# Optimization experiments

Measured on AMD Instinct MI355X. Metric: run time of the kernel, lower is better.

The kernel has to match this reference:

```python
import math
import jax, jax.numpy as jnp
import numpy as np

B, T, C, H = 2, 4096, 512, 8  # batch, seq_len, n_embd, n_head
D = C // H                    # head_dim = 64

def setup_inputs() -> dict:
    key = jax.random.key(0)
    k1, k2, k3 = jax.random.split(key, 3)
    x = jax.random.normal(k1, (B, T, C), dtype=jnp.float32)
    # torch Linear(C, 3C, bias=False): y = x @ W.T; we store the transposed
    # weight directly so the forward is x @ W_attn.
    W_attn = jax.random.normal(k2, (C, 3 * C), dtype=jnp.float32) * 0.02
    W_proj = jax.random.normal(k3, (C, C), dtype=jnp.float32) * 0.02
    return {"x": x, "W_attn": W_attn, "W_proj": W_proj}

def reference(x, W_attn, W_proj):
    b, t, c = x.shape
    # fused QKV projection, split like .split(n_embd, dim=2)
    qkv = x @ W_attn                              # [B,T,3C]
    q, k, v = jnp.split(qkv, 3, axis=-1)          # each [B,T,C]
    def to_heads(u):
        return u.reshape(b, t, H, D).transpose(0, 2, 1, 3)  # [B,H,T,D]
    q, k, v = to_heads(q), to_heads(k), to_heads(v)
    scale = 1.0 / math.sqrt(D)
    att = jnp.einsum('bhqd,bhkd->bhqk', q, k) * scale       # [B,H,T,T]
    causal = jnp.tril(jnp.ones((t, t), dtype=bool))         # masked_fill(triu(...,1), -inf)
    att = jnp.where(causal, att, -jnp.inf)
    probs = jax.nn.softmax(att, axis=-1)
    y = jnp.einsum('bhqk,bhkd->bhqd', probs, v)             # [B,H,T,D]
    y = y.transpose(0, 2, 1, 3).reshape(b, t, c)            # [B,T,C]
    return y @ W_proj
```

## Files before the change

kernel.cpp:

```cpp
#include <hip/hip_runtime.h>
#include <hip/hip_bf16.h>
#include <stdint.h>


typedef __attribute__((ext_vector_type(8))) short short8;
typedef __attribute__((ext_vector_type(4))) float floatx4;

__device__ __forceinline__ unsigned short f2bf(float f) {
    unsigned int x = __float_as_uint(f);
    unsigned int r = x + 0x7fffu + ((x >> 16) & 1u);
    return (unsigned short)(r >> 16);
}

__global__ __launch_bounds__(256) void transpose_w(
    const float* __restrict__ W, unsigned short* __restrict__ Wt, int Kdim, int Ndim)
{
    __shared__ unsigned short tile[32][34];
    const int tid = threadIdx.x;
    const int tx = tid & 31, ty = tid >> 5;
    const int n0 = blockIdx.x * 32, k0 = blockIdx.y * 32;
    #pragma unroll
    for (int p = 0; p < 4; ++p) {
        int k = k0 + ty + p * 8;
        tile[tx][ty + p * 8] = f2bf(W[(size_t)k * Ndim + n0 + tx]);
    }
    __syncthreads();
    #pragma unroll
    for (int p = 0; p < 4; ++p) {
        int n = n0 + ty + p * 8;
        Wt[(size_t)n * Kdim + k0 + tx] = tile[ty + p * 8][tx];
    }
}

template<int EPI, bool AF32>
__global__ __launch_bounds__(256) void mm_bt(
    const void* __restrict__ Ap,
    const unsigned short* __restrict__ Bt,
    void* __restrict__ outp)
{
    __shared__ __align__(16) unsigned short Al[128][40];
    __shared__ __align__(16) unsigned short Bl[128][40];

    const int tid  = threadIdx.x;
    const int wave = tid >> 6;
    const int lane = tid & 63;
    const int quad = lane >> 4;
    const int l16  = lane & 15;
    const int wr   = wave >> 1;
    const int wc   = wave & 1;
    const int n0 = blockIdx.x * 128;
    const int m0 = blockIdx.y * 128;

    floatx4 acc[4][4];
    #pragma unroll
    for (int i = 0; i < 4; ++i)
        #pragma unroll
        for (int j = 0; j < 4; ++j) acc[i][j] = (floatx4){0.f, 0.f, 0.f, 0.f};

    const int row = tid >> 1;
    const int cb  = (tid & 1) * 16;

    for (int k0 = 0; k0 < 512; k0 += 32) {
        __syncthreads();
        if (AF32) {
            const float* src = (const float*)Ap + (size_t)(m0 + row) * 512 + k0 + cb;
            float4 f0 = *reinterpret_cast<const float4*>(src);
            float4 f1 = *reinterpret_cast<const float4*>(src + 4);
            float4 f2 = *reinterpret_cast<const float4*>(src + 8);
            float4 f3 = *reinterpret_cast<const float4*>(src + 12);
            unsigned short o[16] = {
                f2bf(f0.x), f2bf(f0.y), f2bf(f0.z), f2bf(f0.w),
                f2bf(f1.x), f2bf(f1.y), f2bf(f1.z), f2bf(f1.w),
                f2bf(f2.x), f2bf(f2.y), f2bf(f2.z), f2bf(f2.w),
                f2bf(f3.x), f2bf(f3.y), f2bf(f3.z), f2bf(f3.w)};
            *reinterpret_cast<uint4*>(&Al[row][cb])     = reinterpret_cast<uint4*>(o)[0];
            *reinterpret_cast<uint4*>(&Al[row][cb + 8]) = reinterpret_cast<uint4*>(o)[1];
        } else {
            const unsigned short* src = (const unsigned short*)Ap + (size_t)(m0 + row) * 512 + k0 + cb;
            *reinterpret_cast<uint4*>(&Al[row][cb])     = *reinterpret_cast<const uint4*>(src);
            *reinterpret_cast<uint4*>(&Al[row][cb + 8]) = *reinterpret_cast<const uint4*>(src + 8);
        }
        {
            const unsigned short* src = &Bt[(size_t)(n0 + row) * 512 + k0 + cb];
            *reinterpret_cast<uint4*>(&Bl[row][cb])     = *reinterpret_cast<const uint4*>(src);
            *reinterpret_cast<uint4*>(&Bl[row][cb + 8]) = *reinterpret_cast<const uint4*>(src + 8);
        }
        __syncthreads();

        short8 af[4], bf[4];
        #pragma unroll
        for (int ti = 0; ti < 4; ++ti)
            af[ti] = *reinterpret_cast<const short8*>(&Al[wr * 64 + ti * 16 + l16][quad * 8]);
        #pragma unroll
        for (int tj = 0; tj < 4; ++tj)
            bf[tj] = *reinterpret_cast<const short8*>(&Bl[wc * 64 + tj * 16 + l16][quad * 8]);
        #pragma unroll
        for (int ti = 0; ti < 4; ++ti)
            #pragma unroll
            for (int tj = 0; tj < 4; ++tj)
                acc[ti][tj] = __builtin_amdgcn_mfma_f32_16x16x32_bf16(af[ti], bf[tj], acc[ti][tj], 0, 0, 0);
    }

    if (EPI == 0) {
        unsigned short* WS = (unsigned short*)outp;
        unsigned short* Qb  = WS;
        unsigned short* Kb  = WS + 4194304;
        unsigned short* Vtb = WS + 8388608;
        const int which = n0 >> 9;
        const int h = ((n0 + wc * 64) >> 6) & 7;
        const float sc = (which == 0) ? 0.18033688f : 1.0f;
        #pragma unroll
        for (int ti = 0; ti < 4; ++ti) {
            #pragma unroll
            for (int r = 0; r < 4; ++r) {
                int m = m0 + wr * 64 + ti * 16 + quad * 4 + r;
                int b = m >> 12, t = m & 4095;
                int bh = b * 8 + h;
                #pragma unroll
                for (int tj = 0; tj < 4; ++tj) {
                    int d = tj * 16 + l16;
                    unsigned short val = f2bf(acc[ti][tj][r] * sc);
                    if (which == 0)      Qb[((size_t)bh * 4096 + t) * 64 + d] = val;
                    else if (which == 1) Kb[((size_t)bh * 4096 + t) * 64 + d] = val;
                    else                 Vtb[((size_t)bh * 64 + d) * 4096 + t] = val;
                }
            }
        }
    } else {
        float* Out = (float*)outp;
        #pragma unroll
        for (int ti = 0; ti < 4; ++ti) {
            #pragma unroll
            for (int r = 0; r < 4; ++r) {
                int m = m0 + wr * 64 + ti * 16 + quad * 4 + r;
                #pragma unroll
                for (int tj = 0; tj < 4; ++tj) {
                    int n = n0 + wc * 64 + tj * 16 + l16;
                    Out[(size_t)m * 512 + n] = acc[ti][tj][r];
                }
            }
        }
    }
}

__global__ __launch_bounds__(256) void attn_mfma(
    const unsigned short* __restrict__ Q,
    const unsigned short* __restrict__ K,
    const unsigned short* __restrict__ Vt,
    unsigned short* __restrict__ Y)
{
    __shared__ __align__(16) unsigned short Kc[64][72];
    __shared__ __align__(16) unsigned short Vc[64][72];
    __shared__ __align__(16) unsigned short Pc[4][16][72];

    const int tid  = threadIdx.x;
    const int wave = tid >> 6;
    const int lane = tid & 63;
    const int quad = lane >> 4;
    const int l16  = lane & 15;

    const int bid = blockIdx.x;
    const int bh = bid & 15;
    const int j  = (bid >> 4) & 15;
    const int g  = bid >> 8;
    const int qb = (g == 0) ? j : (g == 1) ? (63 - j) : (g == 2) ? (16 + j) : (47 - j);
    const int m0 = qb * 64;

    const unsigned short* Qp = Q  + (size_t)bh * (4096 * 64);
    const unsigned short* Kp = K  + (size_t)bh * (4096 * 64);
    const unsigned short* Vp = Vt + (size_t)bh * (64 * 4096);

    const int qrow = m0 + wave * 16 + l16;
    short8 qf[2];
    qf[0] = *reinterpret_cast<const short8*>(&Qp[(size_t)qrow * 64 + quad * 8]);
    qf[1] = *reinterpret_cast<const short8*>(&Qp[(size_t)qrow * 64 + 32 + quad * 8]);

    short8 ones;
    #pragma unroll
    for (int i = 0; i < 8; ++i) ones[i] = (short)0x3F80;

    floatx4 o[4] = {{0,0,0,0},{0,0,0,0},{0,0,0,0},{0,0,0,0}};
    floatx4 o4 = {0, 0, 0, 0};

    const int r0 = tid >> 3,          c0 = (tid & 7) * 8;
    const int r1 = (tid + 256) >> 3,  c1 = c0;

    uint4 rk0 = *reinterpret_cast<const uint4*>(&Kp[(size_t)r0 * 64 + c0]);
    uint4 rk1 = *reinterpret_cast<const uint4*>(&Kp[(size_t)r1 * 64 + c1]);
    uint4 rv0 = *reinterpret_cast<const uint4*>(&Vp[(size_t)r0 * 4096 + c0]);
    uint4 rv1 = *reinterpret_cast<const uint4*>(&Vp[(size_t)r1 * 4096 + c1]);

    for (int kt = 0; kt <= qb; ++kt) {
        __syncthreads();
        *reinterpret_cast<uint4*>(&Kc[r0][c0]) = rk0;
        *reinterpret_cast<uint4*>(&Kc[r1][c1]) = rk1;
        *reinterpret_cast<uint4*>(&Vc[r0][c0]) = rv0;
        *reinterpret_cast<uint4*>(&Vc[r1][c1]) = rv1;
        __syncthreads();

        if (kt < qb) {
            const int jn = (kt + 1) * 64;
            rk0 = *reinterpret_cast<const uint4*>(&Kp[(size_t)(jn + r0) * 64 + c0]);
            rk1 = *reinterpret_cast<const uint4*>(&Kp[(size_t)(jn + r1) * 64 + c1]);
            rv0 = *reinterpret_cast<const uint4*>(&Vp[(size_t)r0 * 4096 + jn + c0]);
            rv1 = *reinterpret_cast<const uint4*>(&Vp[(size_t)r1 * 4096 + jn + c1]);
        }

        float sv[4][4];
        #pragma unroll
        for (int ct = 0; ct < 4; ++ct) {
            floatx4 s = {0, 0, 0, 0};
            #pragma unroll
            for (int kk = 0; kk < 2; ++kk) {
                short8 a = *reinterpret_cast<const short8*>(&Kc[ct * 16 + l16][kk * 32 + quad * 8]);
                s = __builtin_amdgcn_mfma_f32_16x16x32_bf16(a, qf[kk], s, 0, 0, 0);
            }
            sv[ct][0] = s[0]; sv[ct][1] = s[1]; sv[ct][2] = s[2]; sv[ct][3] = s[3];
        }

        if (kt == qb) {
            #pragma unroll
            for (int ct = 0; ct < 4; ++ct)
                #pragma unroll
                for (int r = 0; r < 4; ++r) {
                    int keyl = ct * 16 + quad * 4 + r;
                    int ql   = wave * 16 + l16;
                    sv[ct][r] = (keyl <= ql) ? sv[ct][r] : -1e30f;
                }
        }
        #pragma unroll
        for (int ct = 0; ct < 4; ++ct)
            #pragma unroll
            for (int r = 0; r < 4; ++r)
                sv[ct][r] = __builtin_amdgcn_exp2f(sv[ct][r]);

        #pragma unroll
        for (int ct = 0; ct < 4; ++ct) {
            unsigned int d0 = (unsigned int)f2bf(sv[ct][0]) | ((unsigned int)f2bf(sv[ct][1]) << 16);
            unsigned int d1 = (unsigned int)f2bf(sv[ct][2]) | ((unsigned int)f2bf(sv[ct][3]) << 16);
            *reinterpret_cast<uint2*>(&Pc[wave][l16][ct * 16 + quad * 4]) = make_uint2(d0, d1);
        }

        short8 pa[2];
        pa[0] = *reinterpret_cast<const short8*>(&Pc[wave][l16][quad * 8]);
        pa[1] = *reinterpret_cast<const short8*>(&Pc[wave][l16][32 + quad * 8]);

        #pragma unroll
        for (int kk = 0; kk < 2; ++kk)
            o4 = __builtin_amdgcn_mfma_f32_16x16x32_bf16(pa[kk], ones, o4, 0, 0, 0);
        #pragma unroll
        for (int n = 0; n < 4; ++n) {
            #pragma unroll
            for (int kk = 0; kk < 2; ++kk) {
                short8 b = *reinterpret_cast<const short8*>(&Vc[n * 16 + l16][kk * 32 + quad * 8]);
                o[n] = __builtin_amdgcn_mfma_f32_16x16x32_bf16(pa[kk], b, o[n], 0, 0, 0);
            }
        }
    }

    const int b = bh >> 3, h = bh & 7;
    #pragma unroll
    for (int r = 0; r < 4; ++r) {
        float inv = 1.0f / o4[r];
        int t = m0 + wave * 16 + quad * 4 + r;
        #pragma unroll
        for (int n = 0; n < 4; ++n)
            Y[((size_t)(b * 4096 + t)) * 512 + h * 64 + n * 16 + l16] = f2bf(o[n][r] * inv);
    }
}

extern "C" void kernel_launch(void* const* d_in, const int* in_sizes, int n_in,
                              void* d_out, int out_size, void* d_ws, size_t ws_size,
                              hipStream_t stream) {
    const float* x  = (const float*)d_in[0];
    const float* Wa = (const float*)d_in[1];
    const float* Wp = (const float*)d_in[2];
    float* out = (float*)d_out;
    unsigned short* ws = (unsigned short*)d_ws;

    unsigned short* Qb  = ws;
    unsigned short* Kb  = ws + 4194304;
    unsigned short* Vtb = ws + 8388608;
    unsigned short* Yb  = ws + 12582912;
    unsigned short* WaT = Yb;
    unsigned short* WpT = Qb;

    dim3 blk(256);
    transpose_w<<<dim3(48, 16), blk, 0, stream>>>(Wa, WaT, 512, 1536);
    mm_bt<0, true><<<dim3(12, 64), blk, 0, stream>>>((const void*)x, WaT, (void*)ws);
    attn_mfma<<<dim3(1024), blk, 0, stream>>>(Qb, Kb, Vtb, Yb);
    transpose_w<<<dim3(16, 16), blk, 0, stream>>>(Wp, WpT, 512, 512);
    mm_bt<1, false><<<dim3(4, 64), blk, 0, stream>>>((const void*)Yb, WpT, (void*)out);
}
```

Before: 190.5 us.

## Enlarge attention query tile, prefetch GEMM tiles, pre-convert x to bf16

The attention kernel now gives each block 128 query rows, with each wave handling 32 rows as two 16-row halves. Every K/V tile loaded into shared memory is reused across twice as many queries, and the grid shrinks to 512 blocks. Waves whose rows lie entirely before a key tile skip its compute. The GEMM now prefetches the next A/B slices into registers while the MFMAs run, and x is converted to bf16 once in a separate kernel, using the output buffer as scratch. The trade-offs are more registers per wave, fewer blocks for load balance under the causal mask, and one extra kernel launch.

```diff
diff --git a/kernel.cpp b/kernel.cpp
--- a/kernel.cpp
+++ b/kernel.cpp
@@ -10,6 +10,17 @@
     unsigned int x = __float_as_uint(f);
     unsigned int r = x + 0x7fffu + ((x >> 16) & 1u);
     return (unsigned short)(r >> 16);
+}
+
+__global__ __launch_bounds__(256) void convert_x(
+    const float* __restrict__ x, unsigned short* __restrict__ xb)
+{
+    size_t i = ((size_t)blockIdx.x * 256 + threadIdx.x) * 8;
+    float4 a = *reinterpret_cast<const float4*>(x + i);
+    float4 b = *reinterpret_cast<const float4*>(x + i + 4);
+    unsigned short o[8] = {f2bf(a.x), f2bf(a.y), f2bf(a.z), f2bf(a.w),
+                           f2bf(b.x), f2bf(b.y), f2bf(b.z), f2bf(b.w)};
+    *reinterpret_cast<uint4*>(xb + i) = *reinterpret_cast<uint4*>(o);
 }
 
 __global__ __launch_bounds__(256) void transpose_w(
@@ -32,9 +43,9 @@
     }
 }
 
-template<int EPI, bool AF32>
+template<int EPI>
 __global__ __launch_bounds__(256) void mm_bt(
-    const void* __restrict__ Ap,
+    const unsigned short* __restrict__ A,
     const unsigned short* __restrict__ Bt,
     void* __restrict__ outp)
 {
@@ -60,32 +71,28 @@
     const int row = tid >> 1;
     const int cb  = (tid & 1) * 16;
 
+    const unsigned short* ap = &A[(size_t)(m0 + row) * 512 + cb];
+    const unsigned short* bp = &Bt[(size_t)(n0 + row) * 512 + cb];
+
+    uint4 ra0 = *reinterpret_cast<const uint4*>(ap);
+    uint4 ra1 = *reinterpret_cast<const uint4*>(ap + 8);
+    uint4 rb0 = *reinterpret_cast<const uint4*>(bp);
+    uint4 rb1 = *reinterpret_cast<const uint4*>(bp + 8);
+
     for (int k0 = 0; k0 < 512; k0 += 32) {
         __syncthreads();
-        if (AF32) {
-            const float* src = (const float*)Ap + (size_t)(m0 + row) * 512 + k0 + cb;
-            float4 f0 = *reinterpret_cast<const float4*>(src);
-            float4 f1 = *reinterpret_cast<const float4*>(src + 4);
-            float4 f2 = *reinterpret_cast<const float4*>(src + 8);
-            float4 f3 = *reinterpret_cast<const float4*>(src + 12);
-            unsigned short o[16] = {
-                f2bf(f0.x), f2bf(f0.y), f2bf(f0.z), f2bf(f0.w),
-                f2bf(f1.x), f2bf(f1.y), f2bf(f1.z), f2bf(f1.w),
-                f2bf(f2.x), f2bf(f2.y), f2bf(f2.z), f2bf(f2.w),
-                f2bf(f3.x), f2bf(f3.y), f2bf(f3.z), f2bf(f3.w)};
-            *reinterpret_cast<uint4*>(&Al[row][cb])     = reinterpret_cast<uint4*>(o)[0];
-            *reinterpret_cast<uint4*>(&Al[row][cb + 8]) = reinterpret_cast<uint4*>(o)[1];
-        } else {
-            const unsigned short* src = (const unsigned short*)Ap + (size_t)(m0 + row) * 512 + k0 + cb;
-            *reinterpret_cast<uint4*>(&Al[row][cb])     = *reinterpret_cast<const uint4*>(src);
-            *reinterpret_cast<uint4*>(&Al[row][cb + 8]) = *reinterpret_cast<const uint4*>(src + 8);
-        }
-        {
-            const unsigned short* src = &Bt[(size_t)(n0 + row) * 512 + k0 + cb];
-            *reinterpret_cast<uint4*>(&Bl[row][cb])     = *reinterpret_cast<const uint4*>(src);
-            *reinterpret_cast<uint4*>(&Bl[row][cb + 8]) = *reinterpret_cast<const uint4*>(src + 8);
-        }
+        *reinterpret_cast<uint4*>(&Al[row][cb])     = ra0;
+        *reinterpret_cast<uint4*>(&Al[row][cb + 8]) = ra1;
+        *reinterpret_cast<uint4*>(&Bl[row][cb])     = rb0;
+        *reinterpret_cast<uint4*>(&Bl[row][cb + 8]) = rb1;
         __syncthreads();
+
+        if (k0 < 480) {
+            ra0 = *reinterpret_cast<const uint4*>(ap + k0 + 32);
+            ra1 = *reinterpret_cast<const uint4*>(ap + k0 + 40);
+            rb0 = *reinterpret_cast<const uint4*>(bp + k0 + 32);
+            rb1 = *reinterpret_cast<const uint4*>(bp + k0 + 40);
+        }
 
         short8 af[4], bf[4];
         #pragma unroll
@@ -151,7 +158,7 @@
 {
     __shared__ __align__(16) unsigned short Kc[64][72];
     __shared__ __align__(16) unsigned short Vc[64][72];
-    __shared__ __align__(16) unsigned short Pc[4][16][72];
+    __shared__ __align__(16) unsigned short Pc[4][32][72];
 
     const int tid  = threadIdx.x;
     const int wave = tid >> 6;
@@ -163,34 +170,43 @@
     const int bh = bid & 15;
     const int j  = (bid >> 4) & 15;
     const int g  = bid >> 8;
-    const int qb = (g == 0) ? j : (g == 1) ? (63 - j) : (g == 2) ? (16 + j) : (47 - j);
-    const int m0 = qb * 64;
+    const int qb = g ? (31 - j) : j;
+    const int m0 = qb * 128;
 
     const unsigned short* Qp = Q  + (size_t)bh * (4096 * 64);
     const unsigned short* Kp = K  + (size_t)bh * (4096 * 64);
     const unsigned short* Vp = Vt + (size_t)bh * (64 * 4096);
 
-    const int qrow = m0 + wave * 16 + l16;
-    short8 qf[2];
-    qf[0] = *reinterpret_cast<const short8*>(&Qp[(size_t)qrow * 64 + quad * 8]);
-    qf[1] = *reinterpret_cast<const short8*>(&Qp[(size_t)qrow * 64 + 32 + quad * 8]);
+    short8 qf[2][2];
+    #pragma unroll
+    for (int h = 0; h < 2; ++h) {
+        int qrow = m0 + wave * 32 + h * 16 + l16;
+        qf[h][0] = *reinterpret_cast<const short8*>(&Qp[(size_t)qrow * 64 + quad * 8]);
+        qf[h][1] = *reinterpret_cast<const short8*>(&Qp[(size_t)qrow * 64 + 32 + quad * 8]);
+    }
 
     short8 ones;
     #pragma unroll
     for (int i = 0; i < 8; ++i) ones[i] = (short)0x3F80;
 
-    floatx4 o[4] = {{0,0,0,0},{0,0,0,0},{0,0,0,0},{0,0,0,0}};
-    floatx4 o4 = {0, 0, 0, 0};
-
-    const int r0 = tid >> 3,          c0 = (tid & 7) * 8;
-    const int r1 = (tid + 256) >> 3,  c1 = c0;
+    floatx4 o[2][4];
+    #pragma unroll
+    for (int h = 0; h < 2; ++h)
+        #pragma unroll
+        for (int n = 0; n < 4; ++n) o[h][n] = (floatx4){0.f, 0.f, 0.f, 0.f};
+    floatx4 o4[2] = {{0,0,0,0},{0,0,0,0}};
+
+    const int r0 = tid >> 3, c0 = (tid & 7) * 8;
+    const int r1 = r0 + 32,  c1 = c0;
+    const int ktmax = 2 * qb + 1;
+    const int wq0 = m0 + wave * 32;
 
     uint4 rk0 = *reinterpret_cast<const uint4*>(&Kp[(size_t)r0 * 64 + c0]);
     uint4 rk1 = *reinterpret_cast<const uint4*>(&Kp[(size_t)r1 * 64 + c1]);
     uint4 rv0 = *reinterpret_cast<const uint4*>(&Vp[(size_t)r0 * 4096 + c0]);
     uint4 rv1 = *reinterpret_cast<const uint4*>(&Vp[(size_t)r1 * 4096 + c1]);
 
-    for (int kt = 0; kt <= qb; ++kt) {
+    for (int kt = 0; kt <= ktmax; ++kt) {
         __syncthreads();
         *reinterpret_cast<uint4*>(&Kc[r0][c0]) = rk0;
         *reinterpret_cast<uint4*>(&Kc[r1][c1]) = rk1;
@@ -198,7 +214,7 @@
         *reinterpret_cast<uint4*>(&Vc[r1][c1]) = rv1;
         __syncthreads();
 
-        if (kt < qb) {
+        if (kt < ktmax) {
             const int jn = (kt + 1) * 64;
             rk0 = *reinterpret_cast<const uint4*>(&Kp[(size_t)(jn + r0) * 64 + c0]);
             rk1 = *reinterpret_cast<const uint4*>(&Kp[(size_t)(jn + r1) * 64 + c1]);
@@ -206,67 +222,86 @@
             rv1 = *reinterpret_cast<const uint4*>(&Vp[(size_t)r1 * 4096 + jn + c1]);
         }
 
-        float sv[4][4];
+        if (kt * 64 > wq0 + 31) continue;
+
+        float sv[2][4][4];
         #pragma unroll
         for (int ct = 0; ct < 4; ++ct) {
-            floatx4 s = {0, 0, 0, 0};
-            #pragma unroll
-            for (int kk = 0; kk < 2; ++kk) {
-                short8 a = *reinterpret_cast<const short8*>(&Kc[ct * 16 + l16][kk * 32 + quad * 8]);
-                s = __builtin_amdgcn_mfma_f32_16x16x32_bf16(a, qf[kk], s, 0, 0, 0);
-            }
-            sv[ct][0] = s[0]; sv[ct][1] = s[1]; sv[ct][2] = s[2]; sv[ct][3] = s[3];
-        }
-
-        if (kt == qb) {
+            short8 a0 = *reinterpret_cast<const short8*>(&Kc[ct * 16 + l16][quad * 8]);
+            short8 a1 = *reinterpret_cast<const short8*>(&Kc[ct * 16 + l16][32 + quad * 8]);
+            floatx4 s0 = {0, 0, 0, 0}, s1 = {0, 0, 0, 0};
+            s0 = __builtin_amdgcn_mfma_f32_16x16x32_bf16(a0, qf[0][0], s0, 0, 0, 0);
+            s0 = __builtin_amdgcn_mfma_f32_16x16x32_bf16(a1, qf[0][1], s0, 0, 0, 0);
+            s1 = __builtin_amdgcn_mfma_f32_16x16x32_bf16(a0, qf[1][0], s1, 0, 0, 0);
+            s1 = __builtin_amdgcn_mfma_f32_16x16x32_bf16(a1, qf[1][1], s1, 0, 0, 0);
+            #pragma unroll
+            for (int r = 0; r < 4; ++r) { sv[0][ct][r] = s0[r]; sv[1][ct][r] = s1[r]; }
+        }
+
+        if (kt * 64 + 63 > wq0) {
+            #pragma unroll
+            for (int h = 0; h < 2; ++h)
+                #pragma unroll
+                for (int ct = 0; ct < 4; ++ct)
+                    #pragma unroll
+                    for (int r = 0; r < 4; ++r) {
+                        int key = kt * 64 + ct * 16 + quad * 4 + r;
+                        int q   = wq0 + h * 16 + l16;
+                        sv[h][ct][r] = (key <= q) ? sv[h][ct][r] : -1e30f;
+                    }
+        }
+        #pragma unroll
+        for (int h = 0; h < 2; ++h)
             #pragma unroll
             for (int ct = 0; ct < 4; ++ct)
                 #pragma unroll
-                for (int r = 0; r < 4; ++r) {
-                    int keyl = ct * 16 + quad * 4 + r;
-                    int ql   = wave * 16 + l16;
-                    sv[ct][r] = (keyl <= ql) ? sv[ct][r] : -1e30f;
-                }
-        }
-        #pragma unroll
-        for (int ct = 0; ct < 4; ++ct)
-            #pragma unroll
-            for (int r = 0; r < 4; ++r)
-                sv[ct][r] = __builtin_amdgcn_exp2f(sv[ct][r]);
-
-        #pragma unroll
-        for (int ct = 0; ct < 4; ++ct) {
-            unsigned int d0 = (unsigned int)f2bf(sv[ct][0]) | ((unsigned int)f2bf(sv[ct][1]) << 16);
-            unsigned int d1 = (unsigned int)f2bf(sv[ct][2]) | ((unsigned int)f2bf(sv[ct][3]) << 16);
-            *reinterpret_cast<uint2*>(&Pc[wave][l16][ct * 16 + quad * 4]) = make_uint2(d0, d1);
-        }
-
-        short8 pa[2];
-        pa[0] = *reinterpret_cast<const short8*>(&Pc[wave][l16][quad * 8]);
-        pa[1] = *reinterpret_cast<const short8*>(&Pc[wave][l16][32 + quad * 8]);
-
-        #pragma unroll
-        for (int kk = 0; kk < 2; ++kk)
-            o4 = __builtin_amdgcn_mfma_f32_16x16x32_bf16(pa[kk], ones, o4, 0, 0, 0);
+                for (int r = 0; r < 4; ++r)
+                    sv[h][ct][r] = __builtin_amdgcn_exp2f(sv[h][ct][r]);
+
+        #pragma unroll
+        for (int h = 0; h < 2; ++h)
+            #pragma unroll
+            for (int ct = 0; ct < 4; ++ct) {
+                unsigned int d0 = (unsigned int)f2bf(sv[h][ct][0]) | ((unsigned int)f2bf(sv[h][ct][1]) << 16);
+                unsigned int d1 = (unsigned int)f2bf(sv[h][ct][2]) | ((unsigned int)f2bf(sv[h][ct][3]) << 16);
+                *reinterpret_cast<uint2*>(&Pc[wave][h * 16 + l16][ct * 16 + quad * 4]) = make_uint2(d0, d1);
+            }
+
+        short8 pa[2][2];
+        #pragma unroll
+        for (int h = 0; h < 2; ++h) {
+            pa[h][0] = *reinterpret_cast<const short8*>(&Pc[wave][h * 16 + l16][quad * 8]);
+            pa[h][1] = *reinterpret_cast<const short8*>(&Pc[wave][h * 16 + l16][32 + quad * 8]);
+        }
+
+        #pragma unroll
+        for (int h = 0; h < 2; ++h) {
+            o4[h] = __builtin_amdgcn_mfma_f32_16x16x32_bf16(pa[h][0], ones, o4[h], 0, 0, 0);
+            o4[h] = __builtin_amdgcn_mfma_f32_16x16x32_bf16(pa[h][1], ones, o4[h], 0, 0, 0);
+        }
         #pragma unroll
         for (int n = 0; n < 4; ++n) {
-            #pragma unroll
-            for (int kk = 0; kk < 2; ++kk) {
-                short8 b = *reinterpret_cast<const short8*>(&Vc[n * 16 + l16][kk * 32 + quad * 8]);
-                o[n] = __builtin_amdgcn_mfma_f32_16x16x32_bf16(pa[kk], b, o[n], 0, 0, 0);
+            short8 b0 = *reinterpret_cast<const short8*>(&Vc[n * 16 + l16][quad * 8]);
+            short8 b1 = *reinterpret_cast<const short8*>(&Vc[n * 16 + l16][32 + quad * 8]);
+            #pragma unroll
+            for (int h = 0; h < 2; ++h) {
+                o[h][n] = __builtin_amdgcn_mfma_f32_16x16x32_bf16(pa[h][0], b0, o[h][n], 0, 0, 0);
+                o[h][n] = __builtin_amdgcn_mfma_f32_16x16x32_bf16(pa[h][1], b1, o[h][n], 0, 0, 0);
             }
         }
     }
 
-    const int b = bh >> 3, h = bh & 7;
-    #pragma unroll
-    for (int r = 0; r < 4; ++r) {
-        float inv = 1.0f / o4[r];
-        int t = m0 + wave * 16 + quad * 4 + r;
-        #pragma unroll
-        for (int n = 0; n < 4; ++n)
-            Y[((size_t)(b * 4096 + t)) * 512 + h * 64 + n * 16 + l16] = f2bf(o[n][r] * inv);
-    }
+    const int b = bh >> 3, h8 = bh & 7;
+    #pragma unroll
+    for (int h = 0; h < 2; ++h)
+        #pragma unroll
+        for (int r = 0; r < 4; ++r) {
+            float inv = 1.0f / o4[h][r];
+            int t = wq0 + h * 16 + quad * 4 + r;
+            #pragma unroll
+            for (int n = 0; n < 4; ++n)
+                Y[((size_t)(b * 4096 + t)) * 512 + h8 * 64 + n * 16 + l16] = f2bf(o[h][n][r] * inv);
+        }
 }
 
 extern "C" void kernel_launch(void* const* d_in, const int* in_sizes, int n_in,
@@ -284,11 +319,13 @@
     unsigned short* Yb  = ws + 12582912;
     unsigned short* WaT = Yb;
     unsigned short* WpT = Qb;
+    unsigned short* xb  = (unsigned short*)d_out;
 
     dim3 blk(256);
+    convert_x<<<dim3(2048), blk, 0, stream>>>(x, xb);
     transpose_w<<<dim3(48, 16), blk, 0, stream>>>(Wa, WaT, 512, 1536);
-    mm_bt<0, true><<<dim3(12, 64), blk, 0, stream>>>((const void*)x, WaT, (void*)ws);
-    attn_mfma<<<dim3(1024), blk, 0, stream>>>(Qb, Kb, Vtb, Yb);
+    mm_bt<0><<<dim3(12, 64), blk, 0, stream>>>(xb, WaT, (void*)ws);
+    attn_mfma<<<dim3(512), blk, 0, stream>>>(Qb, Kb, Vtb, Yb);
     transpose_w<<<dim3(16, 16), blk, 0, stream>>>(Wp, WpT, 512, 512);
-    mm_bt<1, false><<<dim3(4, 64), blk, 0, stream>>>((const void*)Yb, WpT, (void*)out);
-}
+    mm_bt<1><<<dim3(4, 64), blk, 0, stream>>>(Yb, WpT, (void*)out);
+}
```

New measurement: 196.4 us. +3.1%, slower.

## Pre-convert x to bf16, register-prefetch GEMM tiles, LDS-transpose V epilogue

Applied to the files above, without the earlier changes.

Adds a separate kernel that converts x to bf16 into the output buffer, so the QKV GEMM no longer converts fp32 inside its K-loop. Both GEMMs now load the next K-tile into registers while the current tile is multiplied, giving simple software pipelining. The V-transpose epilogue now stages the tile through shared memory and writes coalesced 16-byte rows instead of scattered 2-byte strided stores. This costs one extra launch and a full fp32 read plus bf16 write of x, and the QKV GEMM uses more shared memory for the staging buffer.

```diff
diff --git a/kernel.cpp b/kernel.cpp
--- a/kernel.cpp
+++ b/kernel.cpp
@@ -10,6 +10,17 @@
     unsigned int x = __float_as_uint(f);
     unsigned int r = x + 0x7fffu + ((x >> 16) & 1u);
     return (unsigned short)(r >> 16);
+}
+
+__global__ __launch_bounds__(256) void convert_x(
+    const float* __restrict__ x, unsigned short* __restrict__ xb)
+{
+    size_t i = ((size_t)blockIdx.x * 256 + threadIdx.x) * 8;
+    float4 a = *reinterpret_cast<const float4*>(x + i);
+    float4 b = *reinterpret_cast<const float4*>(x + i + 4);
+    unsigned short o[8] = {f2bf(a.x), f2bf(a.y), f2bf(a.z), f2bf(a.w),
+                           f2bf(b.x), f2bf(b.y), f2bf(b.z), f2bf(b.w)};
+    *reinterpret_cast<uint4*>(xb + i) = *reinterpret_cast<uint4*>(o);
 }
 
 __global__ __launch_bounds__(256) void transpose_w(
@@ -32,14 +43,15 @@
     }
 }
 
-template<int EPI, bool AF32>
+template<int EPI>
 __global__ __launch_bounds__(256) void mm_bt(
-    const void* __restrict__ Ap,
+    const unsigned short* __restrict__ A,
     const unsigned short* __restrict__ Bt,
     void* __restrict__ outp)
 {
-    __shared__ __align__(16) unsigned short Al[128][40];
-    __shared__ __align__(16) unsigned short Bl[128][40];
+    __shared__ __align__(16) unsigned char smem[EPI == 0 ? 40960 : 20480];
+    auto Al = reinterpret_cast<unsigned short(*)[40]>(smem);
+    auto Bl = reinterpret_cast<unsigned short(*)[40]>(smem + 10240);
 
     const int tid  = threadIdx.x;
     const int wave = tid >> 6;
@@ -60,32 +72,28 @@
     const int row = tid >> 1;
     const int cb  = (tid & 1) * 16;
 
+    const unsigned short* ap = &A[(size_t)(m0 + row) * 512 + cb];
+    const unsigned short* bp = &Bt[(size_t)(n0 + row) * 512 + cb];
+
+    uint4 ra0 = *reinterpret_cast<const uint4*>(ap);
+    uint4 ra1 = *reinterpret_cast<const uint4*>(ap + 8);
+    uint4 rb0 = *reinterpret_cast<const uint4*>(bp);
+    uint4 rb1 = *reinterpret_cast<const uint4*>(bp + 8);
+
     for (int k0 = 0; k0 < 512; k0 += 32) {
         __syncthreads();
-        if (AF32) {
-            const float* src = (const float*)Ap + (size_t)(m0 + row) * 512 + k0 + cb;
-            float4 f0 = *reinterpret_cast<const float4*>(src);
-            float4 f1 = *reinterpret_cast<const float4*>(src + 4);
-            float4 f2 = *reinterpret_cast<const float4*>(src + 8);
-            float4 f3 = *reinterpret_cast<const float4*>(src + 12);
-            unsigned short o[16] = {
-                f2bf(f0.x), f2bf(f0.y), f2bf(f0.z), f2bf(f0.w),
-                f2bf(f1.x), f2bf(f1.y), f2bf(f1.z), f2bf(f1.w),
-                f2bf(f2.x), f2bf(f2.y), f2bf(f2.z), f2bf(f2.w),
-                f2bf(f3.x), f2bf(f3.y), f2bf(f3.z), f2bf(f3.w)};
-            *reinterpret_cast<uint4*>(&Al[row][cb])     = reinterpret_cast<uint4*>(o)[0];
-            *reinterpret_cast<uint4*>(&Al[row][cb + 8]) = reinterpret_cast<uint4*>(o)[1];
-        } else {
-            const unsigned short* src = (const unsigned short*)Ap + (size_t)(m0 + row) * 512 + k0 + cb;
-            *reinterpret_cast<uint4*>(&Al[row][cb])     = *reinterpret_cast<const uint4*>(src);
-            *reinterpret_cast<uint4*>(&Al[row][cb + 8]) = *reinterpret_cast<const uint4*>(src + 8);
-        }
-        {
-            const unsigned short* src = &Bt[(size_t)(n0 + row) * 512 + k0 + cb];
-            *reinterpret_cast<uint4*>(&Bl[row][cb])     = *reinterpret_cast<const uint4*>(src);
-            *reinterpret_cast<uint4*>(&Bl[row][cb + 8]) = *reinterpret_cast<const uint4*>(src + 8);
-        }
+        *reinterpret_cast<uint4*>(&Al[row][cb])     = ra0;
+        *reinterpret_cast<uint4*>(&Al[row][cb + 8]) = ra1;
+        *reinterpret_cast<uint4*>(&Bl[row][cb])     = rb0;
+        *reinterpret_cast<uint4*>(&Bl[row][cb + 8]) = rb1;
         __syncthreads();
+
+        if (k0 < 480) {
+            ra0 = *reinterpret_cast<const uint4*>(ap + k0 + 32);
+            ra1 = *reinterpret_cast<const uint4*>(ap + k0 + 40);
+            rb0 = *reinterpret_cast<const uint4*>(bp + k0 + 32);
+            rb1 = *reinterpret_cast<const uint4*>(bp + k0 + 40);
+        }
 
         short8 af[4], bf[4];
         #pragma unroll
@@ -108,21 +116,47 @@
         unsigned short* Vtb = WS + 8388608;
         const int which = n0 >> 9;
         const int h = ((n0 + wc * 64) >> 6) & 7;
-        const float sc = (which == 0) ? 0.18033688f : 1.0f;
-        #pragma unroll
-        for (int ti = 0; ti < 4; ++ti) {
-            #pragma unroll
-            for (int r = 0; r < 4; ++r) {
-                int m = m0 + wr * 64 + ti * 16 + quad * 4 + r;
-                int b = m >> 12, t = m & 4095;
-                int bh = b * 8 + h;
+
+        if (which == 2) {
+            auto Tr = reinterpret_cast<unsigned short(*)[80]>(smem);
+            __syncthreads();
+            #pragma unroll
+            for (int ti = 0; ti < 4; ++ti)
                 #pragma unroll
                 for (int tj = 0; tj < 4; ++tj) {
-                    int d = tj * 16 + l16;
-                    unsigned short val = f2bf(acc[ti][tj][r] * sc);
-                    if (which == 0)      Qb[((size_t)bh * 4096 + t) * 64 + d] = val;
-                    else if (which == 1) Kb[((size_t)bh * 4096 + t) * 64 + d] = val;
-                    else                 Vtb[((size_t)bh * 64 + d) * 4096 + t] = val;
+                    unsigned int lo = (unsigned int)f2bf(acc[ti][tj][0]) |
+                                      ((unsigned int)f2bf(acc[ti][tj][1]) << 16);
+                    unsigned int hi = (unsigned int)f2bf(acc[ti][tj][2]) |
+                                      ((unsigned int)f2bf(acc[ti][tj][3]) << 16);
+                    *reinterpret_cast<uint2*>(&Tr[(wave << 6) + tj * 16 + l16][ti * 16 + quad * 4])
+                        = make_uint2(lo, hi);
+                }
+            const int b = m0 >> 12;
+            const int bh = b * 8 + h;
+            const int t0g = (m0 & 4095) + wr * 64;
+            const int tseg = (lane & 7) * 8;
+            #pragma unroll
+            for (int p = 0; p < 8; ++p) {
+                int dl = p * 8 + (lane >> 3);
+                uint4 v = *reinterpret_cast<const uint4*>(&Tr[(wave << 6) + dl][tseg]);
+                *reinterpret_cast<uint4*>(&Vtb[((size_t)(bh * 64 + dl)) * 4096 + t0g + tseg]) = v;
+            }
+        } else {
+            const float sc = (which == 0) ? 0.18033688f : 1.0f;
+            #pragma unroll
+            for (int ti = 0; ti < 4; ++ti) {
+                #pragma unroll
+                for (int r = 0; r < 4; ++r) {
+                    int m = m0 + wr * 64 + ti * 16 + quad * 4 + r;
+                    int b = m >> 12, t = m & 4095;
+                    int bh = b * 8 + h;
+                    #pragma unroll
+                    for (int tj = 0; tj < 4; ++tj) {
+                        int d = tj * 16 + l16;
+                        unsigned short val = f2bf(acc[ti][tj][r] * sc);
+                        if (which == 0) Qb[((size_t)bh * 4096 + t) * 64 + d] = val;
+                        else            Kb[((size_t)bh * 4096 + t) * 64 + d] = val;
+                    }
                 }
             }
         }
@@ -284,11 +318,13 @@
     unsigned short* Yb  = ws + 12582912;
     unsigned short* WaT = Yb;
     unsigned short* WpT = Qb;
+    unsigned short* xb  = (unsigned short*)d_out;
 
     dim3 blk(256);
+    convert_x<<<dim3(2048), blk, 0, stream>>>(x, xb);
     transpose_w<<<dim3(48, 16), blk, 0, stream>>>(Wa, WaT, 512, 1536);
-    mm_bt<0, true><<<dim3(12, 64), blk, 0, stream>>>((const void*)x, WaT, (void*)ws);
+    mm_bt<0><<<dim3(12, 64), blk, 0, stream>>>(xb, WaT, (void*)ws);
     attn_mfma<<<dim3(1024), blk, 0, stream>>>(Qb, Kb, Vtb, Yb);
     transpose_w<<<dim3(16, 16), blk, 0, stream>>>(Wp, WpT, 512, 512);
-    mm_bt<1, false><<<dim3(4, 64), blk, 0, stream>>>((const void*)Yb, WpT, (void*)out);
-}
+    mm_bt<1><<<dim3(4, 64), blk, 0, stream>>>(Yb, WpT, (void*)out);
+}
```

New measurement: 186.9 us. No clear change (-1.9%).
